# Kernel tuning notes

Measured on AMD Instinct MI355X. Metric: run time of the kernel, lower is better.

The kernel has to match this reference:

```python
import jax, jax.numpy as jnp
import numpy as np

FG_THRESH = 0.5
BG_THRESH_HI = 0.5
BG_THRESH_LO = 0.1


def _bbox_overlaps(boxes, query):
    x1 = jnp.maximum(boxes[:, None, 0], query[None, :, 0])
    y1 = jnp.maximum(boxes[:, None, 1], query[None, :, 1])
    x2 = jnp.minimum(boxes[:, None, 2], query[None, :, 2])
    y2 = jnp.minimum(boxes[:, None, 3], query[None, :, 3])
    iw = jnp.clip(x2 - x1 + 1.0, 0.0)
    ih = jnp.clip(y2 - y1 + 1.0, 0.0)
    inter = iw * ih  # [N,C]
    area_b = (boxes[:, 2] - boxes[:, 0] + 1.0) * (boxes[:, 3] - boxes[:, 1] + 1.0)
    area_q = (query[:, 2] - query[:, 0] + 1.0) * (query[:, 3] - query[:, 1] + 1.0)
    return inter / (area_b[:, None] + area_q[None, :] - inter)


def _refine_supervision(prob, ss_boxes, pos_mask, IS_weight):
    # vectorized, fully on-device version of get_refine_supervision
    C = pos_mask.shape[0]
    p = jax.lax.stop_gradient(prob * IS_weight)  # original detaches via .data.cpu().numpy()
    if p.shape[1] == C + 1:
        p = p[:, 1:]  # drop background column
    max_idx = jnp.argmax(p, axis=0)                     # [C] top-scoring roi per class
    boxes_c = jax.lax.stop_gradient(ss_boxes)[max_idx, 1:5]  # [C,4] pseudo-GT boxes
    ov = _bbox_overlaps(jax.lax.stop_gradient(ss_boxes)[:, 1:5], boxes_c)  # [N,C]
    ov = jnp.where(pos_mask[None, :], ov, -1.0)         # only image-level positive classes
    gt = jnp.argmax(ov, axis=1)                         # [N] assignment
    mo = jnp.max(ov, axis=1)                            # [N] max overlap
    fg = mo > FG_THRESH
    bg = (mo >= BG_THRESH_LO) & (mo < BG_THRESH_HI)
    keep = fg | bg                                      # keep_inds as a mask
    col = jnp.where(fg, gt + 1, 0)                      # one-hot column per kept roi
    return keep, col


def _refine_loss(refine_prob, keep, col, IS_weight):
    n = jnp.sum(keep).astype(refine_prob.dtype)
    lp = jnp.take_along_axis(jnp.log(refine_prob), col[:, None], axis=1)[:, 0]  # [N]
    return -jnp.sum(jnp.where(keep, IS_weight[:, 0] * lp, 0.0)) / n


def reference(fc7_roi, fc7_context, fc7_frame, W_cls, b_cls, W_det, b_det,
              W_r1, b_r1, W_r2, b_r2, ss_boxes, IS_weight, image_level_label):
    C = W_cls.shape[1]
    cls_score = fc7_roi @ W_cls + b_cls                       # [N,C]
    det_score = (fc7_frame @ W_det + b_det) - (fc7_context @ W_det + b_det)  # frame - context
    refine_prob_1 = jax.nn.softmax(fc7_roi @ W_r1 + b_r1, axis=1)  # [N,C+1]
    refine_prob_2 = jax.nn.softmax(fc7_roi @ W_r2 + b_r2, axis=1)
    cls_prob = jax.nn.softmax(cls_score, axis=1)
    det_prob = jax.nn.softmax(det_score, axis=0)              # softmax over rois
    det_cls_prob_product = cls_prob * det_prob                # [N,C]
    det_cls_score = jnp.sum(cls_score * det_prob, axis=0)     # [C]

    pos_mask = image_level_label[0] == 1                      # [C]
    keep1, col1 = _refine_supervision(det_cls_prob_product, ss_boxes, pos_mask, IS_weight)
    refine_loss_1 = _refine_loss(refine_prob_1, keep1, col1, IS_weight)
    keep2, col2 = _refine_supervision(refine_prob_1, ss_boxes, pos_mask, IS_weight)
    refine_loss_2 = _refine_loss(refine_prob_2, keep2, col2, IS_weight)

    lab = image_level_label[0].astype(det_cls_score.dtype)    # +/-1 labels
    cls_det_loss = jnp.sum(jnp.maximum(0.0, 1.0 - lab * det_cls_score)) / C
    total_loss = cls_det_loss + 0.1 * refine_loss_1 + 0.1 * refine_loss_2
    return total_loss


def setup_inputs() -> dict:
    key = jax.random.key(0)
    ks = jax.random.split(key, 16)
    N, F, C = 4096, 4096, 20
    s = 0.01  # weight scale to keep softmax/hinge well-conditioned
    fc7_roi = jax.random.normal(ks[0], (N, F), jnp.float32)
    fc7_context = jax.random.normal(ks[1], (N, F), jnp.float32)
    fc7_frame = jax.random.normal(ks[2], (N, F), jnp.float32)
    W_cls = jax.random.normal(ks[3], (F, C), jnp.float32) * s
    W_det = jax.random.normal(ks[4], (F, C), jnp.float32) * s
    W_r1 = jax.random.normal(ks[5], (F, C + 1), jnp.float32) * s
    W_r2 = jax.random.normal(ks[6], (F, C + 1), jnp.float32) * s
    b_cls = jnp.zeros((C,), jnp.float32)
    b_det = jnp.zeros((C,), jnp.float32)
    b_r1 = jnp.zeros((C + 1,), jnp.float32)
    b_r2 = jnp.zeros((C + 1,), jnp.float32)
    x1 = jax.random.uniform(ks[7], (N,), jnp.float32, 0.0, 500.0)
    y1 = jax.random.uniform(ks[8], (N,), jnp.float32, 0.0, 500.0)
    w = jax.random.uniform(ks[9], (N,), jnp.float32, 10.0, 120.0)
    h = jax.random.uniform(ks[10], (N,), jnp.float32, 10.0, 120.0)
    ss_boxes = jnp.stack([jnp.zeros((N,), jnp.float32), x1, y1, x1 + w, y1 + h], axis=1)
    IS_weight = jax.random.uniform(ks[11], (N, 1), jnp.float32, 0.5, 1.0)
    lbl = jnp.where(jax.random.bernoulli(ks[12], 0.4, (1, C)), 1, -1).astype(jnp.int32)
    lbl = lbl.at[0, 0].set(1)  # guarantee at least one positive class
    return {"fc7_roi": fc7_roi, "fc7_context": fc7_context, "fc7_frame": fc7_frame,
            "W_cls": W_cls, "b_cls": b_cls, "W_det": W_det, "b_det": b_det,
            "W_r1": W_r1, "b_r1": b_r1, "W_r2": W_r2, "b_r2": b_r2,
            "ss_boxes": ss_boxes, "IS_weight": IS_weight, "image_level_label": lbl}
```

## Files before the change

### kernel.cpp

```cpp
#include <hip/hip_runtime.h>

typedef __attribute__((ext_vector_type(4))) float f32x4;
typedef __attribute__((ext_vector_type(8))) short short8;

#define N_ROWS 4096
#define KDIM   4096
#define NC     96
#define NSPLIT 16

__device__ inline short f2bf(float f) {
  unsigned u = __builtin_bit_cast(unsigned, f);
  u += 0x7FFFu + ((u >> 16) & 1u);
  return (short)(u >> 16);
}

__global__ void k_pack(const float* __restrict__ Wcls, const float* __restrict__ Wr1,
                       const float* __restrict__ Wr2, const float* __restrict__ Wdet,
                       ushort* __restrict__ Wp) {
  int t = blockIdx.x * 256 + threadIdx.x;
  int ks = t / 3072;
  int rem = t - ks * 3072;
  int ct = rem >> 9;
  int rem2 = rem & 511;
  int l = rem2 >> 3;
  int j = rem2 & 7;
  int k = ks * 32 + (l >> 4) * 8 + j;
  int col = ct * 16 + (l & 15);
  float v = 0.f;
  if (col < 20)                 v = Wcls[k * 20 + col];
  else if (col < 41)            v = Wr1[k * 21 + (col - 20)];
  else if (col < 62)            v = Wr2[k * 21 + (col - 41)];
  else if (col >= 64 && col < 84) v = Wdet[k * 20 + (col - 64)];
  Wp[t] = (ushort)f2bf(v);
}

__global__ __launch_bounds__(256) void k_gemm(const float* __restrict__ roi,
    const float* __restrict__ frame, const float* __restrict__ ctx,
    const ushort* __restrict__ Wp, float* __restrict__ Spart) {
  const int lane = threadIdx.x & 63;
  const int wid = blockIdx.x * 4 + (threadIdx.x >> 6);
  const int rt = wid & 255;
  const int ks = wid >> 8;
  const int row = rt * 16 + (lane & 15);
  const int kg = lane >> 4;
  const float* pr = roi   + (size_t)row * KDIM;
  const float* pf = frame + (size_t)row * KDIM;
  const float* pc = ctx   + (size_t)row * KDIM;
  f32x4 acc[6];
#pragma unroll
  for (int i = 0; i < 6; ++i) acc[i] = (f32x4){0.f, 0.f, 0.f, 0.f};
  const int s0 = ks * 8;
  for (int s = 0; s < 8; ++s) {
    const int kk = (s0 + s) * 32 + kg * 8;
    f32x4 r0 = *(const f32x4*)(pr + kk);
    f32x4 r1 = *(const f32x4*)(pr + kk + 4);
    f32x4 f0 = *(const f32x4*)(pf + kk);
    f32x4 f1 = *(const f32x4*)(pf + kk + 4);
    f32x4 c0 = *(const f32x4*)(pc + kk);
    f32x4 c1 = *(const f32x4*)(pc + kk + 4);
    short8 aR, aD;
#pragma unroll
    for (int j = 0; j < 4; ++j) {
      aR[j]     = f2bf(r0[j]);
      aR[j + 4] = f2bf(r1[j]);
      aD[j]     = f2bf(f0[j] - c0[j]);
      aD[j + 4] = f2bf(f1[j] - c1[j]);
    }
    const ushort* wb = Wp + ((size_t)(s0 + s) * 6) * 512 + lane * 8;
#pragma unroll
    for (int ct = 0; ct < 6; ++ct) {
      short8 b = *(const short8*)(wb + ct * 512);
      acc[ct] = __builtin_amdgcn_mfma_f32_16x16x32_bf16(ct < 4 ? aR : aD, b, acc[ct], 0, 0, 0);
    }
  }
  float* out = Spart + (size_t)ks * (N_ROWS * NC) + (size_t)rt * 16 * NC;
  const int rbase = (lane >> 4) * 4;
  const int col = lane & 15;
#pragma unroll
  for (int ct = 0; ct < 6; ++ct)
#pragma unroll
    for (int r = 0; r < 4; ++r)
      out[(size_t)(rbase + r) * NC + ct * 16 + col] = acc[ct][r];
}

__global__ void k_reduce(const float* __restrict__ Spart, float* __restrict__ S) {
  int e = blockIdx.x * 256 + threadIdx.x;
  float s = 0.f;
#pragma unroll
  for (int ks = 0; ks < NSPLIT; ++ks) s += Spart[(size_t)ks * (N_ROWS * NC) + e];
  S[e] = s;
}

__global__ void k_rows(const float* __restrict__ S, const float* __restrict__ bcls,
    const float* __restrict__ br1, const float* __restrict__ br2,
    float* __restrict__ clsp, float* __restrict__ rp1,
    float* __restrict__ lse1, float* __restrict__ lse2) {
  int i = blockIdx.x * 256 + threadIdx.x;
  const float* sr = S + (size_t)i * NC;
  float s[21];
  float m = -3.4e38f;
  for (int c = 0; c < 20; ++c) { s[c] = sr[c] + bcls[c]; m = fmaxf(m, s[c]); }
  float sum = 0.f;
  for (int c = 0; c < 20; ++c) { float e = expf(s[c] - m); s[c] = e; sum += e; }
  float inv = 1.f / sum;
  for (int c = 0; c < 20; ++c) clsp[(size_t)i * 20 + c] = s[c] * inv;
  m = -3.4e38f;
  for (int c = 0; c < 21; ++c) { s[c] = sr[20 + c] + br1[c]; m = fmaxf(m, s[c]); }
  sum = 0.f;
  for (int c = 0; c < 21; ++c) { float e = expf(s[c] - m); s[c] = e; sum += e; }
  lse1[i] = m + logf(sum);
  inv = 1.f / sum;
  for (int c = 0; c < 21; ++c) rp1[(size_t)i * 21 + c] = s[c] * inv;
  m = -3.4e38f;
  for (int c = 0; c < 21; ++c) { s[c] = sr[41 + c] + br2[c]; m = fmaxf(m, s[c]); }
  sum = 0.f;
  for (int c = 0; c < 21; ++c) sum += expf(s[c] - m);
  lse2[i] = m + logf(sum);
}

__global__ __launch_bounds__(256) void k_col(const float* __restrict__ S,
    const float* __restrict__ clsp, const float* __restrict__ rp1,
    const float* __restrict__ isw, const float* __restrict__ ssb,
    const float* __restrict__ bcls,
    float* __restrict__ dcs, float* __restrict__ b1out, float* __restrict__ b2out) {
  const int c = blockIdx.x;
  const int t = threadIdx.x;
  __shared__ float rv[256];
  __shared__ int ri[256];
  float m = -3.4e38f;
  for (int i = t; i < N_ROWS; i += 256) m = fmaxf(m, S[(size_t)i * NC + 64 + c]);
  rv[t] = m; __syncthreads();
  for (int o = 128; o; o >>= 1) { if (t < o) rv[t] = fmaxf(rv[t], rv[t + o]); __syncthreads(); }
  const float M = rv[0]; __syncthreads();
  float se = 0.f, scd = 0.f, v1b = -3.4e38f, v2b = -3.4e38f;
  int i1 = 0, i2 = 0;
  for (int i = t; i < N_ROWS; i += 256) {
    float w = isw[i];
    float e = expf(S[(size_t)i * NC + 64 + c] - M);
    se += e;
    scd += (S[(size_t)i * NC + c] + bcls[c]) * e;
    float v1 = clsp[(size_t)i * 20 + c] * e * w;
    if (v1 > v1b) { v1b = v1; i1 = i; }
    float v2 = rp1[(size_t)i * 21 + c + 1] * w;
    if (v2 > v2b) { v2b = v2; i2 = i; }
  }
  rv[t] = se; __syncthreads();
  for (int o = 128; o; o >>= 1) { if (t < o) rv[t] += rv[t + o]; __syncthreads(); }
  const float SE = rv[0]; __syncthreads();
  rv[t] = scd; __syncthreads();
  for (int o = 128; o; o >>= 1) { if (t < o) rv[t] += rv[t + o]; __syncthreads(); }
  const float SCD = rv[0]; __syncthreads();
  rv[t] = v1b; ri[t] = i1; __syncthreads();
  for (int o = 128; o; o >>= 1) {
    if (t < o) { if (rv[t + o] > rv[t] || (rv[t + o] == rv[t] && ri[t + o] < ri[t])) { rv[t] = rv[t + o]; ri[t] = ri[t + o]; } }
    __syncthreads();
  }
  const int I1 = ri[0]; __syncthreads();
  rv[t] = v2b; ri[t] = i2; __syncthreads();
  for (int o = 128; o; o >>= 1) {
    if (t < o) { if (rv[t + o] > rv[t] || (rv[t + o] == rv[t] && ri[t + o] < ri[t])) { rv[t] = rv[t + o]; ri[t] = ri[t + o]; } }
    __syncthreads();
  }
  const int I2 = ri[0];
  if (t == 0) {
    dcs[c] = SCD / SE;
    for (int q = 0; q < 4; ++q) {
      b1out[c * 4 + q] = ssb[(size_t)I1 * 5 + 1 + q];
      b2out[c * 4 + q] = ssb[(size_t)I2 * 5 + 1 + q];
    }
  }
}

__global__ __launch_bounds__(256) void k_sup(const float* __restrict__ S,
    const float* __restrict__ ssb, const float* __restrict__ isw,
    const int* __restrict__ label,
    const float* __restrict__ b1in, const float* __restrict__ b2in,
    const float* __restrict__ lse1, const float* __restrict__ lse2,
    const float* __restrict__ br1, const float* __restrict__ br2,
    float* __restrict__ scal) {
  __shared__ float q1[20][4], q2[20][4], a1[20], a2[20];
  __shared__ int pos[20];
  const int t = threadIdx.x;
  if (t < 20) {
    for (int q = 0; q < 4; ++q) { q1[t][q] = b1in[t * 4 + q]; q2[t][q] = b2in[t * 4 + q]; }
    a1[t] = (q1[t][2] - q1[t][0] + 1.f) * (q1[t][3] - q1[t][1] + 1.f);
    a2[t] = (q2[t][2] - q2[t][0] + 1.f) * (q2[t][3] - q2[t][1] + 1.f);
    pos[t] = (label[t] == 1);
  }
  __syncthreads();
  const int i = blockIdx.x * 256 + t;
  const float bx1 = ssb[(size_t)i * 5 + 1], by1 = ssb[(size_t)i * 5 + 2];
  const float bx2 = ssb[(size_t)i * 5 + 3], by2 = ssb[(size_t)i * 5 + 4];
  const float ab = (bx2 - bx1 + 1.f) * (by2 - by1 + 1.f);
  const float w = isw[i];
  float p1 = 0.f, n1 = 0.f, p2 = 0.f, n2 = 0.f;
  {
    float mo = -2.f; int gt = 0;
    for (int c = 0; c < 20; ++c) {
      float v = -1.f;
      if (pos[c]) {
        float xx1 = fmaxf(bx1, q1[c][0]), yy1 = fmaxf(by1, q1[c][1]);
        float xx2 = fminf(bx2, q1[c][2]), yy2 = fminf(by2, q1[c][3]);
        float iw = fmaxf(xx2 - xx1 + 1.f, 0.f), ih = fmaxf(yy2 - yy1 + 1.f, 0.f);
        float inter = iw * ih;
        v = inter / (ab + a1[c] - inter);
      }
      if (v > mo) { mo = v; gt = c; }
    }
    bool fg = mo > 0.5f;
    bool bg = (mo >= 0.1f) && (mo < 0.5f);
    if (fg || bg) {
      int col = fg ? gt + 1 : 0;
      float lp = S[(size_t)i * NC + 20 + col] + br1[col] - lse1[i];
      p1 = w * lp; n1 = 1.f;
    }
  }
  {
    float mo = -2.f; int gt = 0;
    for (int c = 0; c < 20; ++c) {
      float v = -1.f;
      if (pos[c]) {
        float xx1 = fmaxf(bx1, q2[c][0]), yy1 = fmaxf(by1, q2[c][1]);
        float xx2 = fminf(bx2, q2[c][2]), yy2 = fminf(by2, q2[c][3]);
        float iw = fmaxf(xx2 - xx1 + 1.f, 0.f), ih = fmaxf(yy2 - yy1 + 1.f, 0.f);
        float inter = iw * ih;
        v = inter / (ab + a2[c] - inter);
      }
      if (v > mo) { mo = v; gt = c; }
    }
    bool fg = mo > 0.5f;
    bool bg = (mo >= 0.1f) && (mo < 0.5f);
    if (fg || bg) {
      int col = fg ? gt + 1 : 0;
      float lp = S[(size_t)i * NC + 41 + col] + br2[col] - lse2[i];
      p2 = w * lp; n2 = 1.f;
    }
  }
  __shared__ float rs[256];
  float sums[4] = {p1, n1, p2, n2};
  float tot[4];
  for (int q = 0; q < 4; ++q) {
    rs[t] = sums[q]; __syncthreads();
    for (int o = 128; o; o >>= 1) { if (t < o) rs[t] += rs[t + o]; __syncthreads(); }
    tot[q] = rs[0]; __syncthreads();
  }
  if (t == 0) {
    atomicAdd(&scal[0], tot[0]); atomicAdd(&scal[1], tot[1]);
    atomicAdd(&scal[2], tot[2]); atomicAdd(&scal[3], tot[3]);
  }
}

__global__ void k_final(const float* __restrict__ dcs, const int* __restrict__ label,
                        const float* __restrict__ scal, float* __restrict__ out) {
  if (threadIdx.x == 0 && blockIdx.x == 0) {
    float cd = 0.f;
    for (int c = 0; c < 20; ++c) {
      float lab = (float)label[c];
      cd += fmaxf(1.f - lab * dcs[c], 0.f);
    }
    cd *= (1.f / 20.f);
    float rl1 = -scal[0] / scal[1];
    float rl2 = -scal[2] / scal[3];
    out[0] = cd + 0.1f * (rl1 + rl2);
  }
}

constexpr size_t OFF_S     = 0;
constexpr size_t OFF_SCAL  = OFF_S + (size_t)N_ROWS * NC * 4;
constexpr size_t OFF_DCS   = OFF_SCAL + 16;
constexpr size_t OFF_B1    = OFF_DCS + 80;
constexpr size_t OFF_B2    = OFF_B1 + 320;
constexpr size_t OFF_LSE1  = OFF_B2 + 320;
constexpr size_t OFF_LSE2  = OFF_LSE1 + 16384;
constexpr size_t OFF_CLSP  = OFF_LSE2 + 16384;
constexpr size_t OFF_RP1   = OFF_CLSP + 327680;
constexpr size_t OFF_WP    = OFF_RP1 + 344064;
constexpr size_t OFF_SPART = OFF_WP + 786432;

extern "C" void kernel_launch(void* const* d_in, const int* in_sizes, int n_in,
                              void* d_out, int out_size, void* d_ws, size_t ws_size,
                              hipStream_t stream) {
  const float* roi   = (const float*)d_in[0];
  const float* ctx   = (const float*)d_in[1];
  const float* frame = (const float*)d_in[2];
  const float* Wcls  = (const float*)d_in[3];
  const float* bcls  = (const float*)d_in[4];
  const float* Wdet  = (const float*)d_in[5];
  const float* Wr1   = (const float*)d_in[7];
  const float* br1   = (const float*)d_in[8];
  const float* Wr2   = (const float*)d_in[9];
  const float* br2   = (const float*)d_in[10];
  const float* ssb   = (const float*)d_in[11];
  const float* isw   = (const float*)d_in[12];
  const int*   label = (const int*)d_in[13];

  char* ws = (char*)d_ws;
  float*  S     = (float*)(ws + OFF_S);
  float*  scal  = (float*)(ws + OFF_SCAL);
  float*  dcs   = (float*)(ws + OFF_DCS);
  float*  b1    = (float*)(ws + OFF_B1);
  float*  b2    = (float*)(ws + OFF_B2);
  float*  lse1  = (float*)(ws + OFF_LSE1);
  float*  lse2  = (float*)(ws + OFF_LSE2);
  float*  clsp  = (float*)(ws + OFF_CLSP);
  float*  rp1   = (float*)(ws + OFF_RP1);
  ushort* Wp    = (ushort*)(ws + OFF_WP);
  float*  Spart = (float*)(ws + OFF_SPART);

  hipMemsetAsync(scal, 0, 16, stream);
  k_pack<<<1536, 256, 0, stream>>>(Wcls, Wr1, Wr2, Wdet, Wp);
  k_gemm<<<1024, 256, 0, stream>>>(roi, frame, ctx, Wp, Spart);
  k_reduce<<<1536, 256, 0, stream>>>(Spart, S);
  k_rows<<<16, 256, 0, stream>>>(S, bcls, br1, br2, clsp, rp1, lse1, lse2);
  k_col<<<20, 256, 0, stream>>>(S, clsp, rp1, isw, ssb, bcls, dcs, b1, b2);
  k_sup<<<16, 256, 0, stream>>>(S, ssb, isw, label, b1, b2, lse1, lse2, br1, br2, scal);
  k_final<<<1, 64, 0, stream>>>(dcs, label, scal, (float*)d_out);
}
```

Before: 96.03 us.

## Software-pipeline GEMM A loads with wider per-lane K chunks and repacked weights

Each lane now reads 16 contiguous floats per row, so a K-step spans 64 instead of 32. The weight packing is changed to match that lane-to-K mapping. The A-operand loads for the next chunk are double-buffered in registers and issued before the current chunk's MFMAs, and all B fragments for a chunk are preloaded. Launch bounds now request two blocks per SM, so the extra registers trade against occupancy and may cause spills.

```diff
diff --git a/kernel.cpp b/kernel.cpp
--- a/kernel.cpp
+++ b/kernel.cpp
@@ -18,13 +18,13 @@
                        const float* __restrict__ Wr2, const float* __restrict__ Wdet,
                        ushort* __restrict__ Wp) {
   int t = blockIdx.x * 256 + threadIdx.x;
-  int ks = t / 3072;
-  int rem = t - ks * 3072;
+  int K = t / 3072;
+  int rem = t - K * 3072;
   int ct = rem >> 9;
   int rem2 = rem & 511;
   int l = rem2 >> 3;
   int j = rem2 & 7;
-  int k = ks * 32 + (l >> 4) * 8 + j;
+  int k = (K >> 1) * 64 + (l >> 4) * 16 + (K & 1) * 8 + j;
   int col = ct * 16 + (l & 15);
   float v = 0.f;
   if (col < 20)                 v = Wcls[k * 20 + col];
@@ -34,7 +34,7 @@
   Wp[t] = (ushort)f2bf(v);
 }
 
-__global__ __launch_bounds__(256) void k_gemm(const float* __restrict__ roi,
+__global__ __launch_bounds__(256, 2) void k_gemm(const float* __restrict__ roi,
     const float* __restrict__ frame, const float* __restrict__ ctx,
     const ushort* __restrict__ Wp, float* __restrict__ Spart) {
   const int lane = threadIdx.x & 63;
@@ -43,36 +43,57 @@
   const int ks = wid >> 8;
   const int row = rt * 16 + (lane & 15);
   const int kg = lane >> 4;
-  const float* pr = roi   + (size_t)row * KDIM;
-  const float* pf = frame + (size_t)row * KDIM;
-  const float* pc = ctx   + (size_t)row * KDIM;
+  const size_t aoff = (size_t)row * KDIM + ks * 256 + kg * 16;
+  const float* pr = roi   + aoff;
+  const float* pf = frame + aoff;
+  const float* pc = ctx   + aoff;
+  const ushort* pb = Wp + (size_t)(ks * 8) * 3072 + lane * 8;
+
+  f32x4 A[2][12];
+  short8 Bv[12];
   f32x4 acc[6];
 #pragma unroll
   for (int i = 0; i < 6; ++i) acc[i] = (f32x4){0.f, 0.f, 0.f, 0.f};
-  const int s0 = ks * 8;
-  for (int s = 0; s < 8; ++s) {
-    const int kk = (s0 + s) * 32 + kg * 8;
-    f32x4 r0 = *(const f32x4*)(pr + kk);
-    f32x4 r1 = *(const f32x4*)(pr + kk + 4);
-    f32x4 f0 = *(const f32x4*)(pf + kk);
-    f32x4 f1 = *(const f32x4*)(pf + kk + 4);
-    f32x4 c0 = *(const f32x4*)(pc + kk);
-    f32x4 c1 = *(const f32x4*)(pc + kk + 4);
-    short8 aR, aD;
-#pragma unroll
-    for (int j = 0; j < 4; ++j) {
-      aR[j]     = f2bf(r0[j]);
-      aR[j + 4] = f2bf(r1[j]);
-      aD[j]     = f2bf(f0[j] - c0[j]);
-      aD[j + 4] = f2bf(f1[j] - c1[j]);
-    }
-    const ushort* wb = Wp + ((size_t)(s0 + s) * 6) * 512 + lane * 8;
-#pragma unroll
-    for (int ct = 0; ct < 6; ++ct) {
-      short8 b = *(const short8*)(wb + ct * 512);
-      acc[ct] = __builtin_amdgcn_mfma_f32_16x16x32_bf16(ct < 4 ? aR : aD, b, acc[ct], 0, 0, 0);
-    }
-  }
+
+#pragma unroll
+  for (int q = 0; q < 4; ++q) {
+    A[0][q]     = *(const f32x4*)(pr + q * 4);
+    A[0][4 + q] = *(const f32x4*)(pf + q * 4);
+    A[0][8 + q] = *(const f32x4*)(pc + q * 4);
+  }
+
+#pragma unroll
+  for (int c = 0; c < 4; ++c) {
+#pragma unroll
+    for (int h = 0; h < 2; ++h)
+#pragma unroll
+      for (int ct = 0; ct < 6; ++ct)
+        Bv[h * 6 + ct] = *(const short8*)(pb + (size_t)(c * 2 + h) * 3072 + ct * 512);
+    if (c < 3) {
+#pragma unroll
+      for (int q = 0; q < 4; ++q) {
+        A[(c + 1) & 1][q]     = *(const f32x4*)(pr + (c + 1) * 64 + q * 4);
+        A[(c + 1) & 1][4 + q] = *(const f32x4*)(pf + (c + 1) * 64 + q * 4);
+        A[(c + 1) & 1][8 + q] = *(const f32x4*)(pc + (c + 1) * 64 + q * 4);
+      }
+    }
+#pragma unroll
+    for (int h = 0; h < 2; ++h) {
+      short8 aR, aD;
+#pragma unroll
+      for (int j = 0; j < 8; ++j) {
+        const int q = h * 2 + (j >> 2), e = j & 3;
+        float r = A[c & 1][q][e];
+        float d = A[c & 1][4 + q][e] - A[c & 1][8 + q][e];
+        aR[j] = f2bf(r);
+        aD[j] = f2bf(d);
+      }
+#pragma unroll
+      for (int ct = 0; ct < 6; ++ct)
+        acc[ct] = __builtin_amdgcn_mfma_f32_16x16x32_bf16(ct < 4 ? aR : aD, Bv[h * 6 + ct], acc[ct], 0, 0, 0);
+    }
+  }
+
   float* out = Spart + (size_t)ks * (N_ROWS * NC) + (size_t)rt * 16 * NC;
   const int rbase = (lane >> 4) * 4;
   const int col = lane & 15;
```

Result: slower. 119.6 us (+24.5%).

## Split GEMM K into 32 chunks with manual load pipelining and in-block partial reduction

Applied to the files above, without the earlier changes.

The skinny GEMM now splits K 32 ways with four k-steps per wave. All global loads are issued up front through inline asm and consumed in order behind explicit vmcnt waits, so more bytes are in flight per wave. The four waves of a block reduce their partials in shared memory, which cuts the partial buffer written and later re-read by the reduce kernel from 16 slices to 8. The cost is higher register use per wave (launch_bounds 256,2) and a fragile hand-written wait schedule.

```diff
diff --git a/kernel.cpp b/kernel.cpp
--- a/kernel.cpp
+++ b/kernel.cpp
@@ -6,7 +6,8 @@
 #define N_ROWS 4096
 #define KDIM   4096
 #define NC     96
-#define NSPLIT 16
+#define NSPL   32
+#define NSOUT  8
 
 __device__ inline short f2bf(float f) {
   unsigned u = __builtin_bit_cast(unsigned, f);
@@ -18,13 +19,13 @@
                        const float* __restrict__ Wr2, const float* __restrict__ Wdet,
                        ushort* __restrict__ Wp) {
   int t = blockIdx.x * 256 + threadIdx.x;
-  int ks = t / 3072;
-  int rem = t - ks * 3072;
+  int K = t / 3072;
+  int rem = t - K * 3072;
   int ct = rem >> 9;
   int rem2 = rem & 511;
   int l = rem2 >> 3;
   int j = rem2 & 7;
-  int k = ks * 32 + (l >> 4) * 8 + j;
+  int k = K * 32 + (l >> 4) * 8 + j;
   int col = ct * 16 + (l & 15);
   float v = 0.f;
   if (col < 20)                 v = Wcls[k * 20 + col];
@@ -34,60 +35,87 @@
   Wp[t] = (ushort)f2bf(v);
 }
 
-__global__ __launch_bounds__(256) void k_gemm(const float* __restrict__ roi,
+#define GL(dst, base, OFF) \
+  asm volatile("global_load_dwordx4 %0, %1, off offset:%c2" : "=v"(dst) : "v"(base), "i"(OFF) : "memory")
+#define WAITV(N) asm volatile("s_waitcnt vmcnt(" #N ")" ::: "memory")
+#define SB() __builtin_amdgcn_sched_barrier(0)
+
+#define ISSUE(K) do {                                                  \
+    GL(Ar[K][0], pr, (K)*128);  GL(Ar[K][1], pr, (K)*128 + 16);        \
+    GL(Af[K][0], pf, (K)*128);  GL(Af[K][1], pf, (K)*128 + 16);        \
+    GL(Ac[K][0], pc, (K)*128);  GL(Ac[K][1], pc, (K)*128 + 16);        \
+    const ushort* pbK  = pb + (K)*3072;                                \
+    const ushort* pbK2 = pbK + 2048;                                   \
+    GL(Bv[K][0], pbK, 0);    GL(Bv[K][1], pbK, 1024);                  \
+    GL(Bv[K][2], pbK, 2048); GL(Bv[K][3], pbK, 3072);                  \
+    GL(Bv[K][4], pbK2, 0);   GL(Bv[K][5], pbK2, 1024);                 \
+  } while (0)
+
+#define COMP(K) do {                                                   \
+    short8 aR, aD;                                                     \
+    _Pragma("unroll")                                                  \
+    for (int j = 0; j < 8; ++j) {                                      \
+      const int q = j >> 2, e = j & 3;                                 \
+      aR[j] = f2bf(Ar[K][q][e]);                                       \
+      aD[j] = f2bf(Af[K][q][e] - Ac[K][q][e]);                         \
+    }                                                                  \
+    _Pragma("unroll")                                                  \
+    for (int ct = 0; ct < 6; ++ct)                                     \
+      acc[ct] = __builtin_amdgcn_mfma_f32_16x16x32_bf16(               \
+          ct < 4 ? aR : aD, Bv[K][ct], acc[ct], 0, 0, 0);              \
+  } while (0)
+
+__global__ __launch_bounds__(256, 2) void k_gemm(const float* __restrict__ roi,
     const float* __restrict__ frame, const float* __restrict__ ctx,
     const ushort* __restrict__ Wp, float* __restrict__ Spart) {
   const int lane = threadIdx.x & 63;
-  const int wid = blockIdx.x * 4 + (threadIdx.x >> 6);
-  const int rt = wid & 255;
-  const int ks = wid >> 8;
-  const int row = rt * 16 + (lane & 15);
-  const int kg = lane >> 4;
-  const float* pr = roi   + (size_t)row * KDIM;
-  const float* pf = frame + (size_t)row * KDIM;
-  const float* pc = ctx   + (size_t)row * KDIM;
+  const int wid  = threadIdx.x >> 6;
+  const int g    = blockIdx.x & 7;
+  const int rt   = blockIdx.x >> 3;
+  const int ks   = g * 4 + wid;
+  const int row  = rt * 16 + (lane & 15);
+  const int kg   = lane >> 4;
+  const size_t aoff = (size_t)row * KDIM + ks * 128 + kg * 8;
+  const float* pr = roi   + aoff;
+  const float* pf = frame + aoff;
+  const float* pc = ctx   + aoff;
+  const ushort* pb = Wp + (size_t)ks * 12288 + lane * 8;
+
+  f32x4 Ar[4][2], Af[4][2], Ac[4][2];
+  short8 Bv[4][6];
   f32x4 acc[6];
 #pragma unroll
   for (int i = 0; i < 6; ++i) acc[i] = (f32x4){0.f, 0.f, 0.f, 0.f};
-  const int s0 = ks * 8;
-  for (int s = 0; s < 8; ++s) {
-    const int kk = (s0 + s) * 32 + kg * 8;
-    f32x4 r0 = *(const f32x4*)(pr + kk);
-    f32x4 r1 = *(const f32x4*)(pr + kk + 4);
-    f32x4 f0 = *(const f32x4*)(pf + kk);
-    f32x4 f1 = *(const f32x4*)(pf + kk + 4);
-    f32x4 c0 = *(const f32x4*)(pc + kk);
-    f32x4 c1 = *(const f32x4*)(pc + kk + 4);
-    short8 aR, aD;
-#pragma unroll
-    for (int j = 0; j < 4; ++j) {
-      aR[j]     = f2bf(r0[j]);
-      aR[j + 4] = f2bf(r1[j]);
-      aD[j]     = f2bf(f0[j] - c0[j]);
-      aD[j + 4] = f2bf(f1[j] - c1[j]);
-    }
-    const ushort* wb = Wp + ((size_t)(s0 + s) * 6) * 512 + lane * 8;
-#pragma unroll
-    for (int ct = 0; ct < 6; ++ct) {
-      short8 b = *(const short8*)(wb + ct * 512);
-      acc[ct] = __builtin_amdgcn_mfma_f32_16x16x32_bf16(ct < 4 ? aR : aD, b, acc[ct], 0, 0, 0);
-    }
-  }
-  float* out = Spart + (size_t)ks * (N_ROWS * NC) + (size_t)rt * 16 * NC;
+
+  ISSUE(0); ISSUE(1);
+  ISSUE(2); WAITV(24); SB(); COMP(0);
+  ISSUE(3); WAITV(24); SB(); COMP(1);
+  WAITV(12); SB(); COMP(2);
+  WAITV(0);  SB(); COMP(3);
+
+  __shared__ float red[4 * 16 * NC];
   const int rbase = (lane >> 4) * 4;
   const int col = lane & 15;
 #pragma unroll
   for (int ct = 0; ct < 6; ++ct)
 #pragma unroll
     for (int r = 0; r < 4; ++r)
-      out[(size_t)(rbase + r) * NC + ct * 16 + col] = acc[ct][r];
+      red[(wid * 16 + rbase + r) * NC + ct * 16 + col] = acc[ct][r];
+  __syncthreads();
+  const int t = threadIdx.x;
+  float* outp = Spart + (size_t)g * (N_ROWS * NC) + (size_t)rt * (16 * NC);
+#pragma unroll
+  for (int q = 0; q < 6; ++q) {
+    const int e = t * 6 + q;
+    outp[e] = red[e] + red[1536 + e] + red[3072 + e] + red[4608 + e];
+  }
 }
 
 __global__ void k_reduce(const float* __restrict__ Spart, float* __restrict__ S) {
   int e = blockIdx.x * 256 + threadIdx.x;
   float s = 0.f;
 #pragma unroll
-  for (int ks = 0; ks < NSPLIT; ++ks) s += Spart[(size_t)ks * (N_ROWS * NC) + e];
+  for (int ks = 0; ks < NSOUT; ++ks) s += Spart[(size_t)ks * (N_ROWS * NC) + e];
   S[e] = s;
 }
 
@@ -309,7 +337,7 @@
 
   hipMemsetAsync(scal, 0, 16, stream);
   k_pack<<<1536, 256, 0, stream>>>(Wcls, Wr1, Wr2, Wdet, Wp);
-  k_gemm<<<1024, 256, 0, stream>>>(roi, frame, ctx, Wp, Spart);
+  k_gemm<<<2048, 256, 0, stream>>>(roi, frame, ctx, Wp, Spart);
   k_reduce<<<1536, 256, 0, stream>>>(Spart, S);
   k_rows<<<16, 256, 0, stream>>>(S, bcls, br1, br2, clsp, rp1, lse1, lse2);
   k_col<<<20, 256, 0, stream>>>(S, clsp, rp1, isw, ssb, bcls, dcs, b1, b2);
```

Result: faster. 87.09 us (-9.3%).

## Restructure GEMM with coalesced LDS-staged double buffering and fuse split-K reduce

Applied to the files above, without the earlier changes.

The skinny GEMM is reorganized so each block owns a 16-row tile and a quarter of K. Activations are loaded with coalesced row-contiguous dwordx4 loads, converted to bf16 with packed cvt instructions, and written into a swizzled, double-buffered LDS tile that MFMA reads from. Loads for the next chunk are issued before the current compute, with explicit vmcnt waits, so global latency overlaps with work. The four waves reduce their partial K-sums in LDS, which cuts the global split count from 16 to 4, and the reduce and row-softmax kernels are fused into one launch. In exchange the code depends on hand-written inline asm and manual wait counts, and the fused row kernel runs softmax on only 32 threads per block.

```diff
diff --git a/kernel.cpp b/kernel.cpp
--- a/kernel.cpp
+++ b/kernel.cpp
@@ -2,11 +2,12 @@
 
 typedef __attribute__((ext_vector_type(4))) float f32x4;
 typedef __attribute__((ext_vector_type(8))) short short8;
+typedef __attribute__((ext_vector_type(2))) unsigned int u32x2;
 
 #define N_ROWS 4096
 #define KDIM   4096
 #define NC     96
-#define NSPLIT 16
+#define GSPLIT 4
 
 __device__ inline short f2bf(float f) {
   unsigned u = __builtin_bit_cast(unsigned, f);
@@ -14,17 +15,23 @@
   return (short)(u >> 16);
 }
 
+__device__ inline unsigned cvtpk(float lo, float hi) {
+  unsigned r;
+  asm("v_cvt_pk_bf16_f32 %0, %1, %2" : "=v"(r) : "v"(lo), "v"(hi));
+  return r;
+}
+
 __global__ void k_pack(const float* __restrict__ Wcls, const float* __restrict__ Wr1,
                        const float* __restrict__ Wr2, const float* __restrict__ Wdet,
                        ushort* __restrict__ Wp) {
   int t = blockIdx.x * 256 + threadIdx.x;
-  int ks = t / 3072;
-  int rem = t - ks * 3072;
+  int K = t / 3072;
+  int rem = t - K * 3072;
   int ct = rem >> 9;
   int rem2 = rem & 511;
   int l = rem2 >> 3;
   int j = rem2 & 7;
-  int k = ks * 32 + (l >> 4) * 8 + j;
+  int k = K * 32 + (l >> 4) * 8 + j;
   int col = ct * 16 + (l & 15);
   float v = 0.f;
   if (col < 20)                 v = Wcls[k * 20 + col];
@@ -34,88 +41,160 @@
   Wp[t] = (ushort)f2bf(v);
 }
 
+#define GLo(dst, base, OFF) \
+  asm volatile("global_load_dwordx4 %0, %1, off offset:%c2" : "=v"(dst) : "v"(base), "i"(OFF) : "memory")
+#define WAITV(N) asm volatile("s_waitcnt vmcnt(" #N ")" ::: "memory")
+#define SB() __builtin_amdgcn_sched_barrier(0)
+
 __global__ __launch_bounds__(256) void k_gemm(const float* __restrict__ roi,
     const float* __restrict__ frame, const float* __restrict__ ctx,
     const ushort* __restrict__ Wp, float* __restrict__ Spart) {
-  const int lane = threadIdx.x & 63;
-  const int wid = blockIdx.x * 4 + (threadIdx.x >> 6);
-  const int rt = wid & 255;
-  const int ks = wid >> 8;
-  const int row = rt * 16 + (lane & 15);
-  const int kg = lane >> 4;
-  const float* pr = roi   + (size_t)row * KDIM;
-  const float* pf = frame + (size_t)row * KDIM;
-  const float* pc = ctx   + (size_t)row * KDIM;
+  const int t    = threadIdx.x;
+  const int lane = t & 63;
+  const int seg  = t >> 6;
+  const int rt   = blockIdx.x >> 2;
+  const int g    = blockIdx.x & 3;
+
+  __shared__ alignas(16) char smem[32768];
+
+  const float* pA[3][4];
+#pragma unroll
+  for (int ri = 0; ri < 4; ++ri) {
+    const size_t off = (size_t)(rt * 16 + ri * 4 + seg) * KDIM + g * 1024 + lane * 4;
+    pA[0][ri] = roi + off; pA[1][ri] = frame + off; pA[2][ri] = ctx + off;
+  }
+
+  f32x4 st[12];
+  short8 Bv[2][6];
   f32x4 acc[6];
 #pragma unroll
   for (int i = 0; i < 6; ++i) acc[i] = (f32x4){0.f, 0.f, 0.f, 0.f};
-  const int s0 = ks * 8;
-  for (int s = 0; s < 8; ++s) {
-    const int kk = (s0 + s) * 32 + kg * 8;
-    f32x4 r0 = *(const f32x4*)(pr + kk);
-    f32x4 r1 = *(const f32x4*)(pr + kk + 4);
-    f32x4 f0 = *(const f32x4*)(pf + kk);
-    f32x4 f1 = *(const f32x4*)(pf + kk + 4);
-    f32x4 c0 = *(const f32x4*)(pc + kk);
-    f32x4 c1 = *(const f32x4*)(pc + kk + 4);
-    short8 aR, aD;
-#pragma unroll
-    for (int j = 0; j < 4; ++j) {
-      aR[j]     = f2bf(r0[j]);
-      aR[j + 4] = f2bf(r1[j]);
-      aD[j]     = f2bf(f0[j] - c0[j]);
-      aD[j + 4] = f2bf(f1[j] - c1[j]);
-    }
-    const ushort* wb = Wp + ((size_t)(s0 + s) * 6) * 512 + lane * 8;
-#pragma unroll
-    for (int ct = 0; ct < 6; ++ct) {
-      short8 b = *(const short8*)(wb + ct * 512);
-      acc[ct] = __builtin_amdgcn_mfma_f32_16x16x32_bf16(ct < 4 ? aR : aD, b, acc[ct], 0, 0, 0);
-    }
-  }
-  float* out = Spart + (size_t)ks * (N_ROWS * NC) + (size_t)rt * 16 * NC;
+
+#define STAGE() do {                                                   \
+    _Pragma("unroll") for (int m = 0; m < 3; ++m)                      \
+      _Pragma("unroll") for (int ri = 0; ri < 4; ++ri)                 \
+        GLo(st[m * 4 + ri], pA[m][ri], 0);                             \
+    _Pragma("unroll") for (int m = 0; m < 3; ++m)                      \
+      _Pragma("unroll") for (int ri = 0; ri < 4; ++ri) pA[m][ri] += 256; \
+  } while (0)
+
+#define CONVERT(NB) do {                                               \
+    _Pragma("unroll") for (int ri = 0; ri < 4; ++ri) {                 \
+      const int rw = ri * 4 + seg;                                     \
+      const unsigned ba = ((unsigned)(rw * 512 + lane * 8)) ^ (((unsigned)(rw & 7)) << 4); \
+      f32x4 r = st[ri], f = st[4 + ri], x = st[8 + ri];                \
+      u32x2 vR, vD;                                                    \
+      vR.x = cvtpk(r[0], r[1]); vR.y = cvtpk(r[2], r[3]);              \
+      vD.x = cvtpk(f[0] - x[0], f[1] - x[1]);                          \
+      vD.y = cvtpk(f[2] - x[2], f[3] - x[3]);                          \
+      *(u32x2*)(smem + (NB) * 16384 + ba) = vR;                        \
+      *(u32x2*)(smem + (NB) * 16384 + 8192 + ba) = vD;                 \
+    }                                                                  \
+  } while (0)
+
+#define BLOADS(C) do {                                                 \
+    _Pragma("unroll") for (int h = 0; h < 2; ++h) {                    \
+      const int Kg = g * 32 + (C) * 8 + seg * 2 + h;                   \
+      const ushort* pb  = Wp + (size_t)Kg * 3072 + lane * 8;           \
+      const ushort* pb2 = pb + 2048;                                   \
+      GLo(Bv[h][0], pb, 0);    GLo(Bv[h][1], pb, 1024);                \
+      GLo(Bv[h][2], pb, 2048); GLo(Bv[h][3], pb, 3072);                \
+      GLo(Bv[h][4], pb2, 0);   GLo(Bv[h][5], pb2, 1024);               \
+    }                                                                  \
+  } while (0)
+
+#define COMPUTE(BUF) do {                                              \
+    _Pragma("unroll") for (int h = 0; h < 2; ++h) {                    \
+      const int Kk = seg * 2 + h;                                      \
+      const int rr_ = lane & 15, sub = lane >> 4;                      \
+      const unsigned ra = ((unsigned)(rr_ * 512 + Kk * 64 + sub * 16)) \
+                          ^ (((unsigned)(rr_ & 7)) << 4);              \
+      short8 aR = *(const short8*)(smem + (BUF) * 16384 + ra);         \
+      short8 aD = *(const short8*)(smem + (BUF) * 16384 + 8192 + ra);  \
+      _Pragma("unroll") for (int ct = 0; ct < 6; ++ct)                 \
+        acc[ct] = __builtin_amdgcn_mfma_f32_16x16x32_bf16(             \
+            ct < 4 ? aR : aD, Bv[h][ct], acc[ct], 0, 0, 0);            \
+    }                                                                  \
+  } while (0)
+
+  STAGE();
+  WAITV(0); SB();
+  CONVERT(0);
+  __syncthreads();
+
+#pragma unroll
+  for (int c = 0; c < 4; ++c) {
+    if (c < 3) {
+      BLOADS(c);
+      STAGE();
+      WAITV(12); SB();
+      COMPUTE(c & 1);
+      WAITV(0); SB();
+      CONVERT((c + 1) & 1);
+    } else {
+      BLOADS(c);
+      WAITV(0); SB();
+      COMPUTE(c & 1);
+    }
+    __syncthreads();
+  }
+
+  float* red = (float*)smem;
   const int rbase = (lane >> 4) * 4;
   const int col = lane & 15;
 #pragma unroll
   for (int ct = 0; ct < 6; ++ct)
 #pragma unroll
     for (int r = 0; r < 4; ++r)
-      out[(size_t)(rbase + r) * NC + ct * 16 + col] = acc[ct][r];
-}
-
-__global__ void k_reduce(const float* __restrict__ Spart, float* __restrict__ S) {
-  int e = blockIdx.x * 256 + threadIdx.x;
-  float s = 0.f;
-#pragma unroll
-  for (int ks = 0; ks < NSPLIT; ++ks) s += Spart[(size_t)ks * (N_ROWS * NC) + e];
-  S[e] = s;
-}
-
-__global__ void k_rows(const float* __restrict__ S, const float* __restrict__ bcls,
+      red[(seg * 16 + rbase + r) * NC + ct * 16 + col] = acc[ct][r];
+  __syncthreads();
+  float* outp = Spart + (size_t)g * (N_ROWS * NC) + (size_t)rt * (16 * NC);
+#pragma unroll
+  for (int q = 0; q < 6; ++q) {
+    const int e = t * 6 + q;
+    outp[e] = red[e] + red[1536 + e] + red[3072 + e] + red[4608 + e];
+  }
+}
+
+__global__ void k_rr(const float* __restrict__ Spart, const float* __restrict__ bcls,
     const float* __restrict__ br1, const float* __restrict__ br2,
-    float* __restrict__ clsp, float* __restrict__ rp1,
+    float* __restrict__ S, float* __restrict__ clsp, float* __restrict__ rp1,
     float* __restrict__ lse1, float* __restrict__ lse2) {
-  int i = blockIdx.x * 256 + threadIdx.x;
-  const float* sr = S + (size_t)i * NC;
-  float s[21];
-  float m = -3.4e38f;
-  for (int c = 0; c < 20; ++c) { s[c] = sr[c] + bcls[c]; m = fmaxf(m, s[c]); }
-  float sum = 0.f;
-  for (int c = 0; c < 20; ++c) { float e = expf(s[c] - m); s[c] = e; sum += e; }
-  float inv = 1.f / sum;
-  for (int c = 0; c < 20; ++c) clsp[(size_t)i * 20 + c] = s[c] * inv;
-  m = -3.4e38f;
-  for (int c = 0; c < 21; ++c) { s[c] = sr[20 + c] + br1[c]; m = fmaxf(m, s[c]); }
-  sum = 0.f;
-  for (int c = 0; c < 21; ++c) { float e = expf(s[c] - m); s[c] = e; sum += e; }
-  lse1[i] = m + logf(sum);
-  inv = 1.f / sum;
-  for (int c = 0; c < 21; ++c) rp1[(size_t)i * 21 + c] = s[c] * inv;
-  m = -3.4e38f;
-  for (int c = 0; c < 21; ++c) { s[c] = sr[41 + c] + br2[c]; m = fmaxf(m, s[c]); }
-  sum = 0.f;
-  for (int c = 0; c < 21; ++c) sum += expf(s[c] - m);
-  lse2[i] = m + logf(sum);
+  const int b = blockIdx.x;
+  const int t = threadIdx.x;
+  const int base = b * 3072;
+#pragma unroll
+  for (int j = 0; j < 12; ++j) {
+    const int e = base + j * 256 + t;
+    float s = 0.f;
+#pragma unroll
+    for (int gg = 0; gg < GSPLIT; ++gg) s += Spart[(size_t)gg * (N_ROWS * NC) + e];
+    S[e] = s;
+  }
+  __syncthreads();
+  if (t < 32) {
+    const int i = b * 32 + t;
+    const float* sr = S + (size_t)i * NC;
+    float s[21];
+    float m = -3.4e38f;
+    for (int c = 0; c < 20; ++c) { s[c] = sr[c] + bcls[c]; m = fmaxf(m, s[c]); }
+    float sum = 0.f;
+    for (int c = 0; c < 20; ++c) { float e = expf(s[c] - m); s[c] = e; sum += e; }
+    float inv = 1.f / sum;
+    for (int c = 0; c < 20; ++c) clsp[(size_t)i * 20 + c] = s[c] * inv;
+    m = -3.4e38f;
+    for (int c = 0; c < 21; ++c) { s[c] = sr[20 + c] + br1[c]; m = fmaxf(m, s[c]); }
+    sum = 0.f;
+    for (int c = 0; c < 21; ++c) { float e = expf(s[c] - m); s[c] = e; sum += e; }
+    lse1[i] = m + logf(sum);
+    inv = 1.f / sum;
+    for (int c = 0; c < 21; ++c) rp1[(size_t)i * 21 + c] = s[c] * inv;
+    m = -3.4e38f;
+    for (int c = 0; c < 21; ++c) { s[c] = sr[41 + c] + br2[c]; m = fmaxf(m, s[c]); }
+    sum = 0.f;
+    for (int c = 0; c < 21; ++c) sum += expf(s[c] - m);
+    lse2[i] = m + logf(sum);
+  }
 }
 
 __global__ __launch_bounds__(256) void k_col(const float* __restrict__ S,
@@ -310,8 +389,7 @@
   hipMemsetAsync(scal, 0, 16, stream);
   k_pack<<<1536, 256, 0, stream>>>(Wcls, Wr1, Wr2, Wdet, Wp);
   k_gemm<<<1024, 256, 0, stream>>>(roi, frame, ctx, Wp, Spart);
-  k_reduce<<<1536, 256, 0, stream>>>(Spart, S);
-  k_rows<<<16, 256, 0, stream>>>(S, bcls, br1, br2, clsp, rp1, lse1, lse2);
+  k_rr<<<128, 256, 0, stream>>>(Spart, bcls, br1, br2, S, clsp, rp1, lse1, lse2);
   k_col<<<20, 256, 0, stream>>>(S, clsp, rp1, isw, ssb, bcls, dcs, b1, b2);
   k_sup<<<16, 256, 0, stream>>>(S, ssb, isw, label, b1, b2, lse1, lse2, br1, br2, scal);
   k_final<<<1, 64, 0, stream>>>(dcs, label, scal, (float*)d_out);
```

After: 88.76 us. 1.08x faster.
